# Performance work log

Measured on AMD Instinct MI355X. Metric: run time of the kernel, lower is better.

The kernel has to match this reference:

```python
import jax, jax.numpy as jnp
import numpy as np

N = 100000
IN_CH = 1024
Z = 32
E = 1600000


def _gcn_conv(x, src, dst, W, b, n_nodes):
    # PyG GCNConv: add self-loops, symmetric deg^{-1/2} normalization,
    # message = norm * (x @ W)[src], scatter-add into dst, plus bias.
    loop = jnp.arange(n_nodes)
    s = jnp.concatenate([src, loop])
    d = jnp.concatenate([dst, loop])
    deg = jax.ops.segment_sum(jnp.ones_like(s, dtype=x.dtype), d, num_segments=n_nodes)
    dinv = jnp.where(deg > 0, jax.lax.rsqrt(deg), 0.0)
    norm = dinv[s] * dinv[d]                     # [E+N]
    h = x @ W                                    # [N, out]
    msg = h[s] * norm[:, None]                   # [E+N, out]
    out = jax.ops.segment_sum(msg, d, num_segments=n_nodes)
    return out + b


def setup_inputs() -> dict:
    key = jax.random.key(0)
    ks = jax.random.split(key, 10)
    x = jax.random.normal(ks[0], (N, IN_CH), dtype=jnp.float32)
    edge_index = jax.random.randint(ks[1], (2, E), 0, N, dtype=jnp.int64)
    def lin(k, fan_in, fan_out):
        bound = 1.0 / np.sqrt(fan_in)
        kw, kb = jax.random.split(k)
        W = jax.random.uniform(kw, (fan_in, fan_out), jnp.float32, -bound, bound)
        b = jax.random.uniform(kb, (fan_out,), jnp.float32, -bound, bound)
        return W, b
    Wg1, bg1 = lin(ks[2], IN_CH, 2 * Z)
    Wg2, bg2 = lin(ks[3], 2 * Z, Z)
    Wf1, bf1 = lin(ks[4], Z, 2 * Z)
    Wf2, bf2 = lin(ks[5], 2 * Z, IN_CH)
    return {"x": x, "edge_index": edge_index,
            "Wg1": Wg1, "bg1": bg1, "Wg2": Wg2, "bg2": bg2,
            "Wf1": Wf1, "bf1": bf1, "Wf2": Wf2, "bf2": bf2}


def reference(x, edge_index, Wg1, bg1, Wg2, bg2, Wf1, bf1, Wf2, bf2):
    src, dst = edge_index[0], edge_index[1]
    h = jax.nn.relu(_gcn_conv(x, src, dst, Wg1, bg1, N))
    z = _gcn_conv(h, src, dst, Wg2, bg2, N)          # encode output
    d = jax.nn.relu(z @ Wf1 + bf1)
    out = jax.nn.relu(d @ Wf2 + bf2)                 # decode output
    return out
```

## Files before the change

kernel.cpp:

```cpp
#include <hip/hip_runtime.h>

#define NN 100000
#define EE 1600000

using bf16x8 = __attribute__((ext_vector_type(8))) short;
using f32x4  = __attribute__((ext_vector_type(4))) float;

static __device__ __forceinline__ unsigned short f2bh(float f) {
    unsigned int u = __float_as_uint(f);
    return (unsigned short)((u + 0x7FFFu + ((u >> 16) & 1u)) >> 16);
}
static __device__ __forceinline__ float bh2f(unsigned short h) {
    return __uint_as_float(((unsigned int)h) << 16);
}

static __device__ __forceinline__ void split_pack(float4 a, float4 b,
                                                  bf16x8& h, bf16x8& l) {
    float f[8] = {a.x, a.y, a.z, a.w, b.x, b.y, b.z, b.w};
    union { bf16x8 v; unsigned int u[4]; } H, L;
    #pragma unroll
    for (int e = 0; e < 4; ++e) {
        unsigned int u0 = __float_as_uint(f[2 * e]);
        unsigned int u1 = __float_as_uint(f[2 * e + 1]);
        H.u[e] = (u0 >> 16) | (u1 & 0xFFFF0000u);
        float r0 = f[2 * e]     - __uint_as_float(u0 & 0xFFFF0000u);
        float r1 = f[2 * e + 1] - __uint_as_float(u1 & 0xFFFF0000u);
        L.u[e] = (__float_as_uint(r0) >> 16) | (__float_as_uint(r1) & 0xFFFF0000u);
    }
    h = H.v; l = L.v;
}

__global__ __launch_bounds__(256) void k_init(unsigned int* cursor) {
    int v = blockIdx.x * 256 + threadIdx.x;
    if (v < NN) cursor[v] = 0u;
}

__global__ __launch_bounds__(256) void k_fill(const int* __restrict__ src,
        const int* __restrict__ dst, unsigned int* cursor, int* __restrict__ bkt) {
    int e = blockIdx.x * 256 + threadIdx.x;
    if (e < EE) {
        int d = dst[e];
        unsigned int pos = atomicAdd(&cursor[d], 1u);
        bkt[(size_t)d * 64 + pos] = src[e];
    }
}

__global__ __launch_bounds__(256) void k_dinv(const unsigned int* __restrict__ deg, float* dinv) {
    int v = blockIdx.x * 256 + threadIdx.x;
    if (v < NN) dinv[v] = rsqrtf((float)(deg[v] + 1u));
}

__global__ __launch_bounds__(256) void k_prepW1(const float* __restrict__ W,
        unsigned short* __restrict__ img) {
    int t = blockIdx.x * 256 + threadIdx.x;
    int k = t >> 6, c = t & 63;
    float f = W[k * 64 + c];
    unsigned short h = f2bh(f);
    size_t base = (size_t)(k >> 6) * 9216 + (size_t)c * 72 + (k & 63);
    img[base] = h;
    img[base + 4608] = f2bh(f - bh2f(h));
}

__global__ __launch_bounds__(256) void k_prepW2(const float* __restrict__ W,
        unsigned short* __restrict__ wh, unsigned short* __restrict__ wl) {
    int t = blockIdx.x * 256 + threadIdx.x;
    int k = t >> 10, c = t & 1023;
    float f = W[k * 1024 + c];
    unsigned short h = f2bh(f);
    wh[c * 64 + k] = h;
    wl[c * 64 + k] = f2bh(f - bh2f(h));
}

__global__ __launch_bounds__(256) void k_gemm1(const float* __restrict__ x,
        const unsigned short* __restrict__ wimg,
        const float* __restrict__ dinv, float* __restrict__ g1) {
    __shared__ __align__(16) unsigned short bs[2][2][64][72];
    const int tid = threadIdx.x;
    const int lane = tid & 63, w = tid >> 6;
    const int l16 = lane & 15, g = lane >> 4;
    const int row0 = blockIdx.x * 128 + w * 16;
    const int rA0 = row0 + l16, rA1 = row0 + 64 + l16;
    const bool ok0 = rA0 < NN, ok1 = rA1 < NN;
    const float* xp0 = x + (size_t)rA0 * 1024;
    const float* xp1 = x + (size_t)rA1 * 1024;
    f32x4 acc[2][4] = {};
    {
        const char* gb = (const char*)wimg;
        char* lb = (char*)&bs[0][0][0][0];
        for (int j = w; j < 18; j += 4)
            __builtin_amdgcn_global_load_lds((const unsigned int*)(gb + j * 1024 + lane * 16),
                                             (unsigned int*)(lb + j * 1024), 16, 0, 0);
    }
    __syncthreads();
    int cur = 0;
    for (int t = 0; t < 16; ++t) {
        const int kc = t * 64;
        float4 xr[2][2][2];
        #pragma unroll
        for (int s = 0; s < 2; ++s) {
            const int k0 = kc + s * 32 + g * 8;
            xr[0][s][0] = ok0 ? *(const float4*)(xp0 + k0)     : make_float4(0.f,0.f,0.f,0.f);
            xr[0][s][1] = ok0 ? *(const float4*)(xp0 + k0 + 4) : make_float4(0.f,0.f,0.f,0.f);
            xr[1][s][0] = ok1 ? *(const float4*)(xp1 + k0)     : make_float4(0.f,0.f,0.f,0.f);
            xr[1][s][1] = ok1 ? *(const float4*)(xp1 + k0 + 4) : make_float4(0.f,0.f,0.f,0.f);
        }
        if (t < 15) {
            const char* gb = (const char*)wimg + (size_t)(t + 1) * 18432;
            char* lb = (char*)&bs[cur ^ 1][0][0][0];
            for (int j = w; j < 18; j += 4)
                __builtin_amdgcn_global_load_lds((const unsigned int*)(gb + j * 1024 + lane * 16),
                                                 (unsigned int*)(lb + j * 1024), 16, 0, 0);
        }
        #pragma unroll
        for (int s = 0; s < 2; ++s) {
            bf16x8 ah0, al0, ah1, al1;
            split_pack(xr[0][s][0], xr[0][s][1], ah0, al0);
            split_pack(xr[1][s][0], xr[1][s][1], ah1, al1);
            const int koff = s * 32 + g * 8;
            #pragma unroll
            for (int nf = 0; nf < 4; ++nf) {
                bf16x8 bh = *(const bf16x8*)&bs[cur][0][nf * 16 + l16][koff];
                bf16x8 bl = *(const bf16x8*)&bs[cur][1][nf * 16 + l16][koff];
                acc[0][nf] = __builtin_amdgcn_mfma_f32_16x16x32_bf16(ah0, bh, acc[0][nf], 0, 0, 0);
                acc[1][nf] = __builtin_amdgcn_mfma_f32_16x16x32_bf16(ah1, bh, acc[1][nf], 0, 0, 0);
                acc[0][nf] = __builtin_amdgcn_mfma_f32_16x16x32_bf16(al0, bh, acc[0][nf], 0, 0, 0);
                acc[1][nf] = __builtin_amdgcn_mfma_f32_16x16x32_bf16(al1, bh, acc[1][nf], 0, 0, 0);
                acc[0][nf] = __builtin_amdgcn_mfma_f32_16x16x32_bf16(ah0, bl, acc[0][nf], 0, 0, 0);
                acc[1][nf] = __builtin_amdgcn_mfma_f32_16x16x32_bf16(ah1, bl, acc[1][nf], 0, 0, 0);
            }
        }
        __syncthreads();
        cur ^= 1;
    }
    #pragma unroll
    for (int mf = 0; mf < 2; ++mf) {
        #pragma unroll
        for (int r = 0; r < 4; ++r) {
            int node = row0 + mf * 64 + g * 4 + r;
            if (node < NN) {
                float di = dinv[node];
                #pragma unroll
                for (int nf = 0; nf < 4; ++nf)
                    g1[(size_t)node * 64 + nf * 16 + l16] = acc[mf][nf][r] * di;
            }
        }
    }
}

__global__ __launch_bounds__(256) void k_gather64(const float* __restrict__ g1,
        const int* __restrict__ bkt, const unsigned int* __restrict__ deg,
        const float* __restrict__ dinv, const float* __restrict__ bg1,
        float* __restrict__ h) {
    int wv = (blockIdx.x * 256 + threadIdx.x) >> 6;
    int lane = threadIdx.x & 63;
    if (wv >= NN) return;
    unsigned int n = deg[wv];
    const int* b = bkt + (size_t)wv * 64;
    float sum = g1[(size_t)wv * 64 + lane];
    unsigned int i = 0;
    for (; i + 4 <= n; i += 4) {
        int s0 = b[i], s1 = b[i + 1], s2 = b[i + 2], s3 = b[i + 3];
        float v0 = g1[(size_t)s0 * 64 + lane];
        float v1 = g1[(size_t)s1 * 64 + lane];
        float v2 = g1[(size_t)s2 * 64 + lane];
        float v3 = g1[(size_t)s3 * 64 + lane];
        sum += (v0 + v1) + (v2 + v3);
    }
    for (; i < n; ++i) sum += g1[(size_t)b[i] * 64 + lane];
    h[(size_t)wv * 64 + lane] = fmaxf(sum * dinv[wv] + bg1[lane], 0.f);
}

__global__ __launch_bounds__(256) void k_layer2(const float* __restrict__ h,
        const float* __restrict__ Wg2, const float* __restrict__ dinv,
        float* __restrict__ g2) {
    __shared__ __align__(16) float as[64][68];
    __shared__ __align__(16) float wsh[64][32];
    const int tid = threadIdx.x;
    const int node0 = blockIdx.x * 64;
    {
        const int lr = tid >> 4, lk = (tid & 15) * 4;
        #pragma unroll
        for (int l = 0; l < 4; ++l) {
            int r = lr + l * 16, v = node0 + r;
            float4 a = make_float4(0.f, 0.f, 0.f, 0.f);
            if (v < NN) a = *(const float4*)(h + (size_t)v * 64 + lk);
            *(float4*)&as[r][lk] = a;
        }
        const int wr = tid >> 3, wk = (tid & 7) * 4;
        #pragma unroll
        for (int l = 0; l < 2; ++l) {
            int r = wr + l * 32;
            *(float4*)&wsh[r][wk] = *(const float4*)(Wg2 + (size_t)r * 32 + wk);
        }
    }
    __syncthreads();
    const int tx = tid & 7, ty = tid >> 3;
    float acc[2][4] = {{0.f}};
    for (int kk = 0; kk < 64; kk += 4) {
        float wv[4][4];
        #pragma unroll
        for (int j = 0; j < 4; ++j)
            *(float4*)&wv[j][0] = *(const float4*)&wsh[kk + j][tx * 4];
        #pragma unroll
        for (int i = 0; i < 2; ++i) {
            float xv[4];
            *(float4*)&xv[0] = *(const float4*)&as[ty * 2 + i][kk];
            #pragma unroll
            for (int j = 0; j < 4; ++j) {
                #pragma unroll
                for (int c = 0; c < 4; ++c)
                    acc[i][c] += xv[j] * wv[j][c];
            }
        }
    }
    #pragma unroll
    for (int i = 0; i < 2; ++i) {
        int v = node0 + ty * 2 + i;
        if (v < NN) {
            float di = dinv[v];
            float4 o;
            o.x = acc[i][0] * di; o.y = acc[i][1] * di;
            o.z = acc[i][2] * di; o.w = acc[i][3] * di;
            *(float4*)(g2 + (size_t)v * 32 + tx * 4) = o;
        }
    }
}

__global__ __launch_bounds__(256) void k_gather32(const float* __restrict__ g2,
        const int* __restrict__ bkt, const unsigned int* __restrict__ deg,
        const float* __restrict__ dinv, const float* __restrict__ bg2,
        float* __restrict__ z) {
    int node = (blockIdx.x * 256 + threadIdx.x) >> 5;
    int c = threadIdx.x & 31;
    if (node >= NN) return;
    unsigned int n = deg[node];
    const int* b = bkt + (size_t)node * 64;
    float sum = g2[(size_t)node * 32 + c];
    unsigned int i = 0;
    for (; i + 4 <= n; i += 4) {
        int s0 = b[i], s1 = b[i + 1], s2 = b[i + 2], s3 = b[i + 3];
        float v0 = g2[(size_t)s0 * 32 + c];
        float v1 = g2[(size_t)s1 * 32 + c];
        float v2 = g2[(size_t)s2 * 32 + c];
        float v3 = g2[(size_t)s3 * 32 + c];
        sum += (v0 + v1) + (v2 + v3);
    }
    for (; i < n; ++i) sum += g2[(size_t)b[i] * 32 + c];
    z[(size_t)node * 32 + c] = sum * dinv[node] + bg2[c];
}

__global__ __launch_bounds__(256) void k_decode(const float* __restrict__ z,
        const float* __restrict__ Wf1, const float* __restrict__ bf1,
        const unsigned short* __restrict__ w2hg, const unsigned short* __restrict__ w2lg,
        const float* __restrict__ bf2, float* __restrict__ out) {
    __shared__ __align__(16) unsigned char smem[36864];
    float (*dsh)[68] = (float (*)[68])smem;
    float (*zs)[36]  = (float (*)[36])(smem + 17408);
    float (*w1s)[64] = (float (*)[64])(smem + 17408 + 9216);
    unsigned short (*w2h)[72] = (unsigned short (*)[72])smem;
    unsigned short (*w2l)[72] = (unsigned short (*)[72])(smem + 18432);
    const int tid = threadIdx.x;
    const int lane = tid & 63, w = tid >> 6;
    const int l16 = lane & 15, g = lane >> 4;
    const int node0 = blockIdx.x * 64;

    uint4 ph[4], pl[4];
    #pragma unroll
    for (int j = 0; j < 4; ++j) {
        int fi = tid + 256 * j;
        int c = fi >> 3, k8 = (fi & 7) * 8;
        ph[j] = *(const uint4*)(w2hg + (size_t)c * 64 + k8);
        pl[j] = *(const uint4*)(w2lg + (size_t)c * 64 + k8);
    }

    #pragma unroll
    for (int j = 0; j < 2; ++j) {
        int fi = tid + 256 * j;
        int v = fi >> 3, m4 = (fi & 7) * 4;
        float4 zz = make_float4(0.f, 0.f, 0.f, 0.f);
        if (node0 + v < NN) zz = *(const float4*)(z + (size_t)(node0 + v) * 32 + m4);
        *(float4*)&zs[v][m4] = zz;
    }
    #pragma unroll
    for (int j = 0; j < 2; ++j) {
        int fi = tid + 256 * j;
        int r = fi >> 4, c4 = (fi & 15) * 4;
        *(float4*)&w1s[r][c4] = *(const float4*)(Wf1 + (size_t)r * 64 + c4);
    }
    __syncthreads();

    {
        const int dtx = tid & 15, dty = tid >> 4;
        float acc[4][4] = {{0.f}};
        for (int m = 0; m < 32; m += 4) {
            float wv[4][4];
            #pragma unroll
            for (int j = 0; j < 4; ++j)
                *(float4*)&wv[j][0] = *(const float4*)&w1s[m + j][dtx * 4];
            #pragma unroll
            for (int i = 0; i < 4; ++i) {
                float zv[4];
                *(float4*)&zv[0] = *(const float4*)&zs[dty * 4 + i][m];
                #pragma unroll
                for (int j = 0; j < 4; ++j) {
                    #pragma unroll
                    for (int c = 0; c < 4; ++c)
                        acc[i][c] += zv[j] * wv[j][c];
                }
            }
        }
        float4 b4 = *(const float4*)(bf1 + dtx * 4);
        #pragma unroll
        for (int i = 0; i < 4; ++i) {
            float4 dd;
            dd.x = fmaxf(acc[i][0] + b4.x, 0.f);
            dd.y = fmaxf(acc[i][1] + b4.y, 0.f);
            dd.z = fmaxf(acc[i][2] + b4.z, 0.f);
            dd.w = fmaxf(acc[i][3] + b4.w, 0.f);
            *(float4*)&dsh[dty * 4 + i][dtx * 4] = dd;
        }
    }
    __syncthreads();

    bf16x8 ah[2], al[2];
    {
        int row = w * 16 + l16;
        #pragma unroll
        for (int s = 0; s < 2; ++s) {
            int k0 = s * 32 + g * 8;
            float4 f0 = *(float4*)&dsh[row][k0];
            float4 f1 = *(float4*)&dsh[row][k0 + 4];
            float fv[8] = {f0.x, f0.y, f0.z, f0.w, f1.x, f1.y, f1.z, f1.w};
            bf16x8 hv, lv;
            #pragma unroll
            for (int e = 0; e < 8; ++e) {
                unsigned short hh = f2bh(fv[e]);
                hv[e] = (short)hh;
                lv[e] = (short)f2bh(fv[e] - bh2f(hh));
            }
            ah[s] = hv; al[s] = lv;
        }
    }
    __syncthreads();

    #pragma unroll
    for (int j = 0; j < 4; ++j) {
        int fi = tid + 256 * j;
        int c = fi >> 3, k8 = (fi & 7) * 8;
        *(uint4*)&w2h[c][k8] = ph[j];
        *(uint4*)&w2l[c][k8] = pl[j];
    }
    __syncthreads();

    for (int ch = 0; ch < 8; ++ch) {
        if (ch < 7) {
            const int col0n = (ch + 1) * 128;
            #pragma unroll
            for (int j = 0; j < 4; ++j) {
                int fi = tid + 256 * j;
                int c = fi >> 3, k8 = (fi & 7) * 8;
                ph[j] = *(const uint4*)(w2hg + (size_t)(col0n + c) * 64 + k8);
                pl[j] = *(const uint4*)(w2lg + (size_t)(col0n + c) * 64 + k8);
            }
        }
        const int col0 = ch * 128;
        f32x4 acc[8] = {};
        #pragma unroll
        for (int nf = 0; nf < 8; ++nf) {
            int c = nf * 16 + l16;
            #pragma unroll
            for (int s = 0; s < 2; ++s) {
                int k0 = s * 32 + g * 8;
                bf16x8 bh = *(const bf16x8*)&w2h[c][k0];
                bf16x8 bl = *(const bf16x8*)&w2l[c][k0];
                acc[nf] = __builtin_amdgcn_mfma_f32_16x16x32_bf16(ah[s], bh, acc[nf], 0, 0, 0);
                acc[nf] = __builtin_amdgcn_mfma_f32_16x16x32_bf16(al[s], bh, acc[nf], 0, 0, 0);
                acc[nf] = __builtin_amdgcn_mfma_f32_16x16x32_bf16(ah[s], bl, acc[nf], 0, 0, 0);
            }
        }
        #pragma unroll
        for (int nf = 0; nf < 8; ++nf) {
            int col = col0 + nf * 16 + l16;
            float b = bf2[col];
            #pragma unroll
            for (int r = 0; r < 4; ++r) {
                int node = node0 + w * 16 + g * 4 + r;
                if (node < NN)
                    out[(size_t)node * 1024 + col] = fmaxf(acc[nf][r] + b, 0.f);
            }
        }
        __syncthreads();
        if (ch < 7) {
            #pragma unroll
            for (int j = 0; j < 4; ++j) {
                int fi = tid + 256 * j;
                int c = fi >> 3, k8 = (fi & 7) * 8;
                *(uint4*)&w2h[c][k8] = ph[j];
                *(uint4*)&w2l[c][k8] = pl[j];
            }
            __syncthreads();
        }
    }
}

extern "C" void kernel_launch(void* const* d_in, const int* in_sizes, int n_in,
                              void* d_out, int out_size, void* d_ws, size_t ws_size,
                              hipStream_t stream) {
    const float* x   = (const float*)d_in[0];
    const int* ei    = (const int*)d_in[1];
    const float* Wg1 = (const float*)d_in[2];
    const float* bg1 = (const float*)d_in[3];
    const float* Wg2 = (const float*)d_in[4];
    const float* bg2 = (const float*)d_in[5];
    const float* Wf1 = (const float*)d_in[6];
    const float* bf1 = (const float*)d_in[7];
    const float* Wf2 = (const float*)d_in[8];
    const float* bf2 = (const float*)d_in[9];
    float* out = (float*)d_out;
    float* ws  = (float*)d_ws;

    const int* src = ei;
    const int* dst = ei + EE;

    float* dinv = ws;
    float* g2   = ws + NN;
    float* z    = ws + NN + 32 * NN;
    unsigned short* wf2h = (unsigned short*)g2;
    unsigned short* wf2l = wf2h + 64 * 1024;

    float* g1 = out;
    float* h  = out + (size_t)64 * NN;
    int* bkt  = (int*)(out + (size_t)128 * NN);
    unsigned int* cursor = (unsigned int*)(bkt + (size_t)64 * NN);
    unsigned short* wg1img = (unsigned short*)(cursor + NN);

    k_init  <<<(NN + 255) / 256, 256, 0, stream>>>(cursor);
    k_fill  <<<(EE + 255) / 256, 256, 0, stream>>>(src, dst, cursor, bkt);
    k_dinv  <<<(NN + 255) / 256, 256, 0, stream>>>(cursor, dinv);
    k_prepW1<<<256, 256, 0, stream>>>(Wg1, wg1img);
    k_gemm1 <<<(NN + 127) / 128, 256, 0, stream>>>(x, wg1img, dinv, g1);
    k_gather64<<<(NN * 64 + 255) / 256, 256, 0, stream>>>(g1, bkt, cursor, dinv, bg1, h);
    k_layer2<<<(NN + 63) / 64, 256, 0, stream>>>(h, Wg2, dinv, g2);
    k_gather32<<<(NN * 32 + 255) / 256, 256, 0, stream>>>(g2, bkt, cursor, dinv, bg2, z);
    k_prepW2<<<256, 256, 0, stream>>>(Wf2, wf2h, wf2l);
    k_decode<<<(NN + 63) / 64, 256, 0, stream>>>(z, Wf1, bf1, wf2h, wf2l, bf2, out);
}
```

Before: 700.1 us.

## Shrink gemm1 tiles with register-prefetched x, stage decode output through LDS

The first GEMM now uses 64-row blocks and 32-wide K chunks, with a smaller LDS weight image, and prefetches the next x slice into registers while computing the current one. This is meant to raise occupancy and overlap the dominant x read with the MFMA work. The decode kernel processes 64-column chunks, prefetches weights two chunks ahead, and stages results in LDS so each row is written to global memory as contiguous float4 stores instead of scattered scalar stores. The cost is more loop iterations and barriers per block, and less data reuse per block in gemm1.

```diff
diff --git a/kernel.cpp b/kernel.cpp
--- a/kernel.cpp
+++ b/kernel.cpp
@@ -56,9 +56,10 @@
     int k = t >> 6, c = t & 63;
     float f = W[k * 64 + c];
     unsigned short h = f2bh(f);
-    size_t base = (size_t)(k >> 6) * 9216 + (size_t)c * 72 + (k & 63);
+    int chunk = k >> 5, kk = k & 31;
+    size_t base = (size_t)chunk * 4608 + (size_t)c * 36 + kk;
     img[base] = h;
-    img[base + 4608] = f2bh(f - bh2f(h));
+    img[base + 2304] = f2bh(f - bh2f(h));
 }
 
 __global__ __launch_bounds__(256) void k_prepW2(const float* __restrict__ W,
@@ -74,75 +75,55 @@
 __global__ __launch_bounds__(256) void k_gemm1(const float* __restrict__ x,
         const unsigned short* __restrict__ wimg,
         const float* __restrict__ dinv, float* __restrict__ g1) {
-    __shared__ __align__(16) unsigned short bs[2][2][64][72];
+    __shared__ __align__(16) unsigned short bs[2][2][64][36];
     const int tid = threadIdx.x;
     const int lane = tid & 63, w = tid >> 6;
     const int l16 = lane & 15, g = lane >> 4;
-    const int row0 = blockIdx.x * 128 + w * 16;
-    const int rA0 = row0 + l16, rA1 = row0 + 64 + l16;
-    const bool ok0 = rA0 < NN, ok1 = rA1 < NN;
-    const float* xp0 = x + (size_t)rA0 * 1024;
-    const float* xp1 = x + (size_t)rA1 * 1024;
-    f32x4 acc[2][4] = {};
-    {
-        const char* gb = (const char*)wimg;
-        char* lb = (char*)&bs[0][0][0][0];
-        for (int j = w; j < 18; j += 4)
-            __builtin_amdgcn_global_load_lds((const unsigned int*)(gb + j * 1024 + lane * 16),
-                                             (unsigned int*)(lb + j * 1024), 16, 0, 0);
-    }
+    const int row0 = blockIdx.x * 64;
+    const int rA = row0 + w * 16 + l16;
+    const bool okA = rA < NN;
+    const float* xp = x + (size_t)rA * 1024 + g * 8;
+    const char* wb = (const char*)wimg;
+    f32x4 acc[4] = {};
+    for (int j = w; j < 9; j += 4)
+        __builtin_amdgcn_global_load_lds((const unsigned int*)(wb + j * 1024 + lane * 16),
+                                         (unsigned int*)((char*)&bs[0][0][0][0] + j * 1024), 16, 0, 0);
+    float4 xr0 = make_float4(0.f,0.f,0.f,0.f), xr1 = xr0;
+    if (okA) { xr0 = *(const float4*)(xp); xr1 = *(const float4*)(xp + 4); }
     __syncthreads();
     int cur = 0;
-    for (int t = 0; t < 16; ++t) {
-        const int kc = t * 64;
-        float4 xr[2][2][2];
-        #pragma unroll
-        for (int s = 0; s < 2; ++s) {
-            const int k0 = kc + s * 32 + g * 8;
-            xr[0][s][0] = ok0 ? *(const float4*)(xp0 + k0)     : make_float4(0.f,0.f,0.f,0.f);
-            xr[0][s][1] = ok0 ? *(const float4*)(xp0 + k0 + 4) : make_float4(0.f,0.f,0.f,0.f);
-            xr[1][s][0] = ok1 ? *(const float4*)(xp1 + k0)     : make_float4(0.f,0.f,0.f,0.f);
-            xr[1][s][1] = ok1 ? *(const float4*)(xp1 + k0 + 4) : make_float4(0.f,0.f,0.f,0.f);
-        }
-        if (t < 15) {
-            const char* gb = (const char*)wimg + (size_t)(t + 1) * 18432;
+    for (int t = 0; t < 32; ++t) {
+        float4 nx0 = make_float4(0.f,0.f,0.f,0.f), nx1 = nx0;
+        if (t < 31) {
+            const char* gb = wb + (size_t)(t + 1) * 9216;
             char* lb = (char*)&bs[cur ^ 1][0][0][0];
-            for (int j = w; j < 18; j += 4)
+            for (int j = w; j < 9; j += 4)
                 __builtin_amdgcn_global_load_lds((const unsigned int*)(gb + j * 1024 + lane * 16),
                                                  (unsigned int*)(lb + j * 1024), 16, 0, 0);
-        }
-        #pragma unroll
-        for (int s = 0; s < 2; ++s) {
-            bf16x8 ah0, al0, ah1, al1;
-            split_pack(xr[0][s][0], xr[0][s][1], ah0, al0);
-            split_pack(xr[1][s][0], xr[1][s][1], ah1, al1);
-            const int koff = s * 32 + g * 8;
-            #pragma unroll
-            for (int nf = 0; nf < 4; ++nf) {
-                bf16x8 bh = *(const bf16x8*)&bs[cur][0][nf * 16 + l16][koff];
-                bf16x8 bl = *(const bf16x8*)&bs[cur][1][nf * 16 + l16][koff];
-                acc[0][nf] = __builtin_amdgcn_mfma_f32_16x16x32_bf16(ah0, bh, acc[0][nf], 0, 0, 0);
-                acc[1][nf] = __builtin_amdgcn_mfma_f32_16x16x32_bf16(ah1, bh, acc[1][nf], 0, 0, 0);
-                acc[0][nf] = __builtin_amdgcn_mfma_f32_16x16x32_bf16(al0, bh, acc[0][nf], 0, 0, 0);
-                acc[1][nf] = __builtin_amdgcn_mfma_f32_16x16x32_bf16(al1, bh, acc[1][nf], 0, 0, 0);
-                acc[0][nf] = __builtin_amdgcn_mfma_f32_16x16x32_bf16(ah0, bl, acc[0][nf], 0, 0, 0);
-                acc[1][nf] = __builtin_amdgcn_mfma_f32_16x16x32_bf16(ah1, bl, acc[1][nf], 0, 0, 0);
-            }
+            if (okA) { nx0 = *(const float4*)(xp + (t + 1) * 32);
+                       nx1 = *(const float4*)(xp + (t + 1) * 32 + 4); }
+        }
+        bf16x8 ah, al;
+        split_pack(xr0, xr1, ah, al);
+        #pragma unroll
+        for (int nf = 0; nf < 4; ++nf) {
+            bf16x8 bh = *(const bf16x8*)&bs[cur][0][nf * 16 + l16][g * 8];
+            bf16x8 bl = *(const bf16x8*)&bs[cur][1][nf * 16 + l16][g * 8];
+            acc[nf] = __builtin_amdgcn_mfma_f32_16x16x32_bf16(ah, bh, acc[nf], 0, 0, 0);
+            acc[nf] = __builtin_amdgcn_mfma_f32_16x16x32_bf16(al, bh, acc[nf], 0, 0, 0);
+            acc[nf] = __builtin_amdgcn_mfma_f32_16x16x32_bf16(ah, bl, acc[nf], 0, 0, 0);
         }
         __syncthreads();
-        cur ^= 1;
-    }
-    #pragma unroll
-    for (int mf = 0; mf < 2; ++mf) {
-        #pragma unroll
-        for (int r = 0; r < 4; ++r) {
-            int node = row0 + mf * 64 + g * 4 + r;
-            if (node < NN) {
-                float di = dinv[node];
-                #pragma unroll
-                for (int nf = 0; nf < 4; ++nf)
-                    g1[(size_t)node * 64 + nf * 16 + l16] = acc[mf][nf][r] * di;
-            }
+        xr0 = nx0; xr1 = nx1; cur ^= 1;
+    }
+    #pragma unroll
+    for (int r = 0; r < 4; ++r) {
+        int node = row0 + w * 16 + g * 4 + r;
+        if (node < NN) {
+            float di = dinv[node];
+            #pragma unroll
+            for (int nf = 0; nf < 4; ++nf)
+                g1[(size_t)node * 64 + nf * 16 + l16] = acc[nf][r] * di;
         }
     }
 }
@@ -253,20 +234,21 @@
         const float* __restrict__ Wf1, const float* __restrict__ bf1,
         const unsigned short* __restrict__ w2hg, const unsigned short* __restrict__ w2lg,
         const float* __restrict__ bf2, float* __restrict__ out) {
-    __shared__ __align__(16) unsigned char smem[36864];
+    __shared__ __align__(16) unsigned char smem[35328];
     float (*dsh)[68] = (float (*)[68])smem;
     float (*zs)[36]  = (float (*)[36])(smem + 17408);
-    float (*w1s)[64] = (float (*)[64])(smem + 17408 + 9216);
+    float (*w1s)[64] = (float (*)[64])(smem + 26624);
     unsigned short (*w2h)[72] = (unsigned short (*)[72])smem;
-    unsigned short (*w2l)[72] = (unsigned short (*)[72])(smem + 18432);
+    unsigned short (*w2l)[72] = (unsigned short (*)[72])(smem + 9216);
+    float (*ost)[66] = (float (*)[66])(smem + 18432);
     const int tid = threadIdx.x;
     const int lane = tid & 63, w = tid >> 6;
     const int l16 = lane & 15, g = lane >> 4;
     const int node0 = blockIdx.x * 64;
 
-    uint4 ph[4], pl[4];
-    #pragma unroll
-    for (int j = 0; j < 4; ++j) {
+    uint4 ph[2], pl[2];
+    #pragma unroll
+    for (int j = 0; j < 2; ++j) {
         int fi = tid + 256 * j;
         int c = fi >> 3, k8 = (fi & 7) * 8;
         ph[j] = *(const uint4*)(w2hg + (size_t)c * 64 + k8);
@@ -344,29 +326,21 @@
     __syncthreads();
 
     #pragma unroll
-    for (int j = 0; j < 4; ++j) {
+    for (int j = 0; j < 2; ++j) {
         int fi = tid + 256 * j;
         int c = fi >> 3, k8 = (fi & 7) * 8;
         *(uint4*)&w2h[c][k8] = ph[j];
         *(uint4*)&w2l[c][k8] = pl[j];
-    }
-    __syncthreads();
-
-    for (int ch = 0; ch < 8; ++ch) {
-        if (ch < 7) {
-            const int col0n = (ch + 1) * 128;
-            #pragma unroll
-            for (int j = 0; j < 4; ++j) {
-                int fi = tid + 256 * j;
-                int c = fi >> 3, k8 = (fi & 7) * 8;
-                ph[j] = *(const uint4*)(w2hg + (size_t)(col0n + c) * 64 + k8);
-                pl[j] = *(const uint4*)(w2lg + (size_t)(col0n + c) * 64 + k8);
-            }
-        }
-        const int col0 = ch * 128;
-        f32x4 acc[8] = {};
-        #pragma unroll
-        for (int nf = 0; nf < 8; ++nf) {
+        ph[j] = *(const uint4*)(w2hg + (size_t)(64 + c) * 64 + k8);
+        pl[j] = *(const uint4*)(w2lg + (size_t)(64 + c) * 64 + k8);
+    }
+    __syncthreads();
+
+    for (int ch = 0; ch < 16; ++ch) {
+        const int col0 = ch * 64;
+        f32x4 acc[4] = {};
+        #pragma unroll
+        for (int nf = 0; nf < 4; ++nf) {
             int c = nf * 16 + l16;
             #pragma unroll
             for (int s = 0; s < 2; ++s) {
@@ -379,27 +353,37 @@
             }
         }
         #pragma unroll
-        for (int nf = 0; nf < 8; ++nf) {
-            int col = col0 + nf * 16 + l16;
-            float b = bf2[col];
-            #pragma unroll
-            for (int r = 0; r < 4; ++r) {
-                int node = node0 + w * 16 + g * 4 + r;
-                if (node < NN)
-                    out[(size_t)node * 1024 + col] = fmaxf(acc[nf][r] + b, 0.f);
-            }
+        for (int nf = 0; nf < 4; ++nf) {
+            float b = bf2[col0 + nf * 16 + l16];
+            #pragma unroll
+            for (int r = 0; r < 4; ++r)
+                ost[w * 16 + g * 4 + r][nf * 16 + l16] = fmaxf(acc[nf][r] + b, 0.f);
         }
         __syncthreads();
-        if (ch < 7) {
-            #pragma unroll
-            for (int j = 0; j < 4; ++j) {
+        if (ch < 15) {
+            #pragma unroll
+            for (int j = 0; j < 2; ++j) {
                 int fi = tid + 256 * j;
                 int c = fi >> 3, k8 = (fi & 7) * 8;
                 *(uint4*)&w2h[c][k8] = ph[j];
                 *(uint4*)&w2l[c][k8] = pl[j];
-            }
-            __syncthreads();
-        }
+                if (ch < 14) {
+                    ph[j] = *(const uint4*)(w2hg + (size_t)((ch + 2) * 64 + c) * 64 + k8);
+                    pl[j] = *(const uint4*)(w2lg + (size_t)((ch + 2) * 64 + c) * 64 + k8);
+                }
+            }
+        }
+        #pragma unroll
+        for (int j = 0; j < 4; ++j) {
+            int fi = tid + 256 * j;
+            int row = fi >> 4, c4 = (fi & 15) * 4;
+            int node = node0 + row;
+            if (node < NN) {
+                float4 o = *(float4*)&ost[row][c4];
+                *(float4*)(out + (size_t)node * 1024 + col0 + c4) = o;
+            }
+        }
+        __syncthreads();
     }
 }
 
@@ -438,7 +422,7 @@
     k_fill  <<<(EE + 255) / 256, 256, 0, stream>>>(src, dst, cursor, bkt);
     k_dinv  <<<(NN + 255) / 256, 256, 0, stream>>>(cursor, dinv);
     k_prepW1<<<256, 256, 0, stream>>>(Wg1, wg1img);
-    k_gemm1 <<<(NN + 127) / 128, 256, 0, stream>>>(x, wg1img, dinv, g1);
+    k_gemm1 <<<(NN + 63) / 64, 256, 0, stream>>>(x, wg1img, dinv, g1);
     k_gather64<<<(NN * 64 + 255) / 256, 256, 0, stream>>>(g1, bkt, cursor, dinv, bg1, h);
     k_layer2<<<(NN + 63) / 64, 256, 0, stream>>>(h, Wg2, dinv, g2);
     k_gather32<<<(NN * 32 + 255) / 256, 256, 0, stream>>>(g2, bkt, cursor, dinv, bg2, z);
```

Result: faster. 609.1 us (-13.0%).
